# Kernel tuning notes

Hardware: AMD Instinct MI355X
Metric: run time of the kernel (lower is better)

## Reference

```python
import jax, jax.numpy as jnp
import numpy as np

N, E, D, OUT, H, R = 50000, 800000, 64, 64, 4, 32
NEG_SLOPE = 0.2  # GATConv default negative_slope


def setup_inputs() -> dict:
    key = jax.random.key(0)
    ks = jax.random.split(key, 10)
    s = 0.05
    return {
        "x": jax.random.normal(ks[0], (N, D), jnp.float32),
        "edge_index": jax.random.randint(ks[1], (2, E), 0, N, jnp.int32),
        "edge_type": jax.random.randint(ks[2], (E,), 0, R, jnp.int32),
        "rel_emb": jax.random.normal(ks[3], (R, D), jnp.float32) * s,   # nn.Embedding weight
        "W": jax.random.normal(ks[4], (D, H * OUT), jnp.float32) * s,   # GATConv.lin (no bias)
        "W_e": jax.random.normal(ks[5], (D, H * OUT), jnp.float32) * s, # GATConv.lin_edge
        "att_src": jax.random.normal(ks[6], (H, OUT), jnp.float32) * s,
        "att_dst": jax.random.normal(ks[7], (H, OUT), jnp.float32) * s,
        "att_edge": jax.random.normal(ks[8], (H, OUT), jnp.float32) * s,
        "bias": jnp.zeros((OUT,), jnp.float32),
    }


def reference(x, edge_index, edge_type, rel_emb, W, W_e, att_src, att_dst, att_edge, bias):
    src, dst = edge_index[0], edge_index[1]
    # per-head node transform: [N, H, C]
    xh = (x @ W).reshape(N, H, OUT)
    a_src = jnp.einsum("nhc,hc->nh", xh, att_src)  # [N, H]
    a_dst = jnp.einsum("nhc,hc->nh", xh, att_dst)  # [N, H]
    # relational edge embedding lookup + edge transform: [E, H, C]
    eh = (rel_emb[edge_type] @ W_e).reshape(E, H, OUT)
    a_edge = jnp.einsum("ehc,hc->eh", eh, att_edge)  # [E, H]
    # raw attention logits per edge, per head
    alpha = jax.nn.leaky_relu(a_src[src] + a_dst[dst] + a_edge, NEG_SLOPE)
    # segment softmax over incoming edges of each destination node
    m = jax.ops.segment_max(alpha, dst, num_segments=N)
    ex = jnp.exp(alpha - m[dst])
    denom = jax.ops.segment_sum(ex, dst, num_segments=N)
    att = ex / denom[dst]  # [E, H]  (dropout disabled: eval mode)
    # weighted scatter-aggregate of source features
    out = jax.ops.segment_sum(xh[src] * att[:, :, None], dst, num_segments=N)  # [N, H, C]
    # concat=False -> mean over heads, then bias
    return out.mean(axis=1) + bias
```

## Files before the change

### kernel.cpp

```cpp
#include <hip/hip_runtime.h>
#include <hip/hip_fp16.h>

#define N_NODES 50000
#define N_EDGES 800000
#define NREL 32
#define NEG_SLOPE 0.2f
#define SCAN_NB ((N_NODES + 255) / 256)
#define HIST_NB ((N_EDGES + 255) / 256)
#define NXB 256
#define NTILES (N_NODES / 16)

typedef _Float16 f16x8 __attribute__((ext_vector_type(8)));
typedef float f32x4 __attribute__((ext_vector_type(4)));

__global__ __launch_bounds__(64) void prep_kernel(
    const float* __restrict__ rel_emb, const float* __restrict__ W_e,
    const float* __restrict__ att_edge, float* __restrict__ a_edge_r,
    const float* __restrict__ W, const float* __restrict__ att_src,
    const float* __restrict__ att_dst, float* __restrict__ vsd)
{
    int tid = threadIdx.x;
    if (blockIdx.x < NREL) {
        int r = blockIdx.x;
        int h = tid >> 4;
        int i16 = tid & 15;
        float rr = rel_emb[r * 64 + tid];
        float4 acc = {0.f, 0.f, 0.f, 0.f};
        #pragma unroll
        for (int k = 0; k < 64; ++k) {
            float rv = __shfl(rr, k);
            float4 wv = *(const float4*)(W_e + k * 256 + h * 64 + i16 * 4);
            acc.x += rv * wv.x; acc.y += rv * wv.y;
            acc.z += rv * wv.z; acc.w += rv * wv.w;
        }
        float4 aev = *(const float4*)(att_edge + h * 64 + i16 * 4);
        float ae = acc.x * aev.x + acc.y * aev.y + acc.z * aev.z + acc.w * aev.w;
        #pragma unroll
        for (int m = 8; m >= 1; m >>= 1) ae += __shfl_xor(ae, m);
        if (i16 == 0) a_edge_r[r * 4 + h] = ae;
    } else {
        int col8 = blockIdx.x - NREL;
        int h = col8 >> 1;
        const float* att = (col8 & 1) ? att_dst : att_src;
        int k = tid;
        float s = 0.f;
        #pragma unroll 8
        for (int c = 0; c < 64; ++c)
            s += W[k * 256 + h * 64 + c] * att[h * 64 + c];
        vsd[col8 * 64 + k] = s;
    }
}

__global__ __launch_bounds__(256) void nx_mfma(
    const float* __restrict__ x, const float* __restrict__ W,
    const float* __restrict__ vsd, __half* __restrict__ xh,
    float* __restrict__ a_src, float* __restrict__ a_dst)
{
    __shared__ __align__(16) _Float16 Wl[272][72];
    int tid = threadIdx.x;

    for (int idx = tid; idx < 64 * 256; idx += 256) {
        int k = idx >> 8, col = idx & 255;
        Wl[col][k] = (_Float16)W[idx];
    }
    for (int idx = tid; idx < 64 * 16; idx += 256) {
        int k = idx >> 4, col8 = idx & 15;
        Wl[256 + col8][k] = (_Float16)((col8 < 8) ? vsd[col8 * 64 + k] : 0.f);
    }
    __syncthreads();

    int lane = tid & 63;
    int wv = tid >> 6;
    int r16 = lane & 15;
    int kg = lane >> 4;

    for (int tile = blockIdx.x * 4 + wv; tile < NTILES; tile += NXB * 4) {
        int nb = tile * 16;
        const float* __restrict__ xrow = x + (size_t)(nb + r16) * 64 + kg * 8;
        float4 u0 = *(const float4*)(xrow);
        float4 u1 = *(const float4*)(xrow + 4);
        float4 u2 = *(const float4*)(xrow + 32);
        float4 u3 = *(const float4*)(xrow + 36);
        f16x8 A0, A1;
        A0[0] = (_Float16)u0.x; A0[1] = (_Float16)u0.y;
        A0[2] = (_Float16)u0.z; A0[3] = (_Float16)u0.w;
        A0[4] = (_Float16)u1.x; A0[5] = (_Float16)u1.y;
        A0[6] = (_Float16)u1.z; A0[7] = (_Float16)u1.w;
        A1[0] = (_Float16)u2.x; A1[1] = (_Float16)u2.y;
        A1[2] = (_Float16)u2.z; A1[3] = (_Float16)u2.w;
        A1[4] = (_Float16)u3.x; A1[5] = (_Float16)u3.y;
        A1[6] = (_Float16)u3.z; A1[7] = (_Float16)u3.w;

        f32x4 D[17];
        #pragma unroll
        for (int ct = 0; ct < 17; ++ct) {
            f16x8 B0 = *(const f16x8*)&Wl[ct * 16 + r16][kg * 8];
            f16x8 B1 = *(const f16x8*)&Wl[ct * 16 + r16][32 + kg * 8];
            f32x4 d = {0.f, 0.f, 0.f, 0.f};
            d = __builtin_amdgcn_mfma_f32_16x16x32_f16(A0, B0, d, 0, 0, 0);
            d = __builtin_amdgcn_mfma_f32_16x16x32_f16(A1, B1, d, 0, 0, 0);
            D[ct] = d;
        }

        #pragma unroll
        for (int r = 0; r < 4; ++r) {
            int n = nb + kg * 4 + r;
            #pragma unroll
            for (int j = 0; j < 4; ++j) {
                __half2 lo = __floats2half2_rn(D[j][r], D[j + 4][r]);
                __half2 hi = __floats2half2_rn(D[j + 8][r], D[j + 12][r]);
                uint2 pk;
                pk.x = *(unsigned int*)&lo;
                pk.y = *(unsigned int*)&hi;
                *(uint2*)(xh + (size_t)n * 256 + (j * 16 + r16) * 4) = pk;
            }
            if (r16 < 8) {
                float v = D[16][r];
                int h = r16 >> 1;
                if (r16 & 1) a_dst[n * 4 + h] = v;
                else         a_src[n * 4 + h] = v;
            }
        }
    }
}

__global__ __launch_bounds__(256) void hist_kernel(const int* __restrict__ ei,
                                                   int* __restrict__ counts,
                                                   int* __restrict__ rank) {
    int e = blockIdx.x * 256 + threadIdx.x;
    if (e < N_EDGES) rank[e] = atomicAdd(&counts[ei[N_EDGES + e]], 1);
}

__global__ __launch_bounds__(256) void scan1_kernel(const int* __restrict__ counts,
                                                    int* __restrict__ offsets,
                                                    int* __restrict__ blocksums) {
    __shared__ int sh[256];
    int tid = threadIdx.x;
    int i = blockIdx.x * 256 + tid;
    int v = (i < N_NODES) ? counts[i] : 0;
    sh[tid] = v;
    __syncthreads();
    #pragma unroll
    for (int off = 1; off < 256; off <<= 1) {
        int t = (tid >= off) ? sh[tid - off] : 0;
        __syncthreads();
        sh[tid] += t;
        __syncthreads();
    }
    if (i < N_NODES) offsets[i] = sh[tid] - v;
    if (tid == 255) blocksums[blockIdx.x] = sh[255];
}

__global__ __launch_bounds__(256) void scan23_kernel(int* __restrict__ offsets,
                                                     const int* __restrict__ blocksums) {
    __shared__ int wsum[4];
    int tid = threadIdx.x;
    int lane = tid & 63;
    int warp = tid >> 6;

    int v = (tid < SCAN_NB && tid < (int)blockIdx.x) ? blocksums[tid] : 0;
    #pragma unroll
    for (int m = 32; m >= 1; m >>= 1) v += __shfl_xor(v, m);
    if (lane == 0) wsum[warp] = v;
    __syncthreads();
    int boff = wsum[0] + wsum[1] + wsum[2] + wsum[3];

    int i = blockIdx.x * 256 + tid;
    if (i < N_NODES) offsets[i] += boff;
}

__global__ __launch_bounds__(256) void scatter_kernel(const int* __restrict__ ei,
                                                      const int* __restrict__ etype,
                                                      const int* __restrict__ offsets,
                                                      const int* __restrict__ rank,
                                                      int* __restrict__ elist) {
    int e = blockIdx.x * 256 + threadIdx.x;
    if (e >= N_EDGES) return;
    int s = ei[e];
    int d = ei[N_EDGES + e];
    int t = etype[e];
    int pos = offsets[d] + rank[e];
    elist[pos] = (s << 5) | t;
}

__global__ __launch_bounds__(256) void aggregate(
    const int* __restrict__ offsets, const int* __restrict__ counts,
    const int* __restrict__ elist, const float* __restrict__ a_src,
    const float* __restrict__ a_dst, const float* __restrict__ a_edge_r,
    const __half* __restrict__ xh, const float* __restrict__ bias,
    float* __restrict__ out)
{
    __shared__ float4 exsh[4][64];
    __shared__ int    ssh[4][64];
    __shared__ float4 pnum[4][64];
    __shared__ float4 pden[4][64];

    int lane = threadIdx.x & 63;
    int warp = threadIdx.x >> 6;
    int pair = warp >> 1;
    int half = warp & 1;
    int d = blockIdx.x * 2 + pair;

    int beg = offsets[d];
    int deg = counts[d];
    int h1 = (deg + 1) >> 1;
    int mybeg = beg + (half ? h1 : 0);
    int mydeg = half ? (deg - h1) : h1;

    float4 advec = ((const float4*)a_dst)[d];

    float n0 = 0.f, n1 = 0.f, n2 = 0.f, n3 = 0.f;
    float d0 = 0.f, d1 = 0.f, d2 = 0.f, d3 = 0.f;

    for (int base = 0; base < mydeg; base += 64) {
        int m = mydeg - base; if (m > 64) m = 64;

        float4 ev = make_float4(0.f, 0.f, 0.f, 0.f);
        int s = 0;
        if (lane < m) {
            int pk = elist[mybeg + base + lane];
            s = pk >> 5;
            int t = pk & 31;
            float4 as = ((const float4*)a_src)[s];
            float4 ae = ((const float4*)a_edge_r)[t];
            float b0 = as.x + advec.x + ae.x; b0 = b0 > 0.f ? b0 : NEG_SLOPE * b0;
            float b1 = as.y + advec.y + ae.y; b1 = b1 > 0.f ? b1 : NEG_SLOPE * b1;
            float b2 = as.z + advec.z + ae.z; b2 = b2 > 0.f ? b2 : NEG_SLOPE * b2;
            float b3 = as.w + advec.w + ae.w; b3 = b3 > 0.f ? b3 : NEG_SLOPE * b3;
            ev.x = __expf(b0); ev.y = __expf(b1);
            ev.z = __expf(b2); ev.w = __expf(b3);
        }
        d0 += ev.x; d1 += ev.y; d2 += ev.z; d3 += ev.w;
        exsh[warp][lane] = ev;
        ssh[warp][lane]  = s;

        #pragma unroll 4
        for (int j = 0; j < m; ++j) {
            float4 e = exsh[warp][j];
            int sj = ssh[warp][j];
            const __half2* __restrict__ xr =
                (const __half2*)(xh + (size_t)sj * 256 + lane * 4);
            __half2 p0 = xr[0], p1 = xr[1];
            float2 f0 = __half22float2(p0), f1 = __half22float2(p1);
            n0 = fmaf(e.x, f0.x, n0);
            n1 = fmaf(e.y, f0.y, n1);
            n2 = fmaf(e.z, f1.x, n2);
            n3 = fmaf(e.w, f1.y, n3);
        }
    }

    pnum[warp][lane] = make_float4(n0, n1, n2, n3);
    pden[warp][lane] = make_float4(d0, d1, d2, d3);
    __syncthreads();

    if (half == 0) {
        float4 on = pnum[warp + 1][lane];
        float4 od = pden[warp + 1][lane];
        n0 += on.x; n1 += on.y; n2 += on.z; n3 += on.w;
        d0 += od.x; d1 += od.y; d2 += od.z; d3 += od.w;

        #pragma unroll
        for (int msk = 32; msk >= 1; msk >>= 1) {
            d0 += __shfl_xor(d0, msk);
            d1 += __shfl_xor(d1, msk);
            d2 += __shfl_xor(d2, msk);
            d3 += __shfl_xor(d3, msk);
        }

        float r = 0.f;
        if (deg > 0)
            r = 0.25f * (n0 / d0 + n1 / d1 + n2 / d2 + n3 / d3);
        out[(size_t)d * 64 + lane] = r + bias[lane];
    }
}

extern "C" void kernel_launch(void* const* d_in, const int* in_sizes, int n_in,
                              void* d_out, int out_size, void* d_ws, size_t ws_size,
                              hipStream_t stream) {
    const float* x        = (const float*)d_in[0];
    const int*   ei       = (const int*)  d_in[1];
    const int*   etype    = (const int*)  d_in[2];
    const float* rel_emb  = (const float*)d_in[3];
    const float* W        = (const float*)d_in[4];
    const float* W_e      = (const float*)d_in[5];
    const float* att_src  = (const float*)d_in[6];
    const float* att_dst  = (const float*)d_in[7];
    const float* att_edge = (const float*)d_in[8];
    const float* bias     = (const float*)d_in[9];
    float* out = (float*)d_out;

    char* ws = (char*)d_ws;
    __half* xh      = (__half*)ws;
    char* p = ws + (size_t)N_NODES * 256 * 2;
    int*   counts   = (int*)p;                p += N_NODES * 4;
    float* a_src    = (float*)p;              p += N_NODES * 4 * 4;
    float* a_dst    = (float*)p;              p += N_NODES * 4 * 4;
    float* a_edge_r = (float*)p;              p += NREL * 4 * 4;
    float* vsd      = (float*)p;              p += 8 * 64 * 4;
    int*   offsets  = (int*)p;                p += N_NODES * 4;
    int*   blocksums= (int*)p;                p += 256 * 4;
    int*   rank     = (int*)p;                p += (size_t)N_EDGES * 4;
    int*   elist    = (int*)p;                p += (size_t)N_EDGES * 4;

    hipMemsetAsync(counts, 0, N_NODES * sizeof(int), stream);
    prep_kernel<<<NREL + 8, 64, 0, stream>>>(rel_emb, W_e, att_edge, a_edge_r,
                                             W, att_src, att_dst, vsd);
    nx_mfma<<<NXB, 256, 0, stream>>>(x, W, vsd, xh, a_src, a_dst);
    hist_kernel<<<HIST_NB, 256, 0, stream>>>(ei, counts, rank);
    scan1_kernel<<<SCAN_NB, 256, 0, stream>>>(counts, offsets, blocksums);
    scan23_kernel<<<SCAN_NB, 256, 0, stream>>>(offsets, blocksums);
    scatter_kernel<<<HIST_NB, 256, 0, stream>>>(ei, etype, offsets, rank, elist);
    aggregate<<<N_NODES / 2, 256, 0, stream>>>(offsets, counts, elist, a_src,
                                               a_dst, a_edge_r, xh, bias, out);
}
```

Before: 153.2 us.

## Merge prep, node transform and histogram into one heterogeneous kernel

```diff
diff --git a/kernel.cpp b/kernel.cpp
--- a/kernel.cpp
+++ b/kernel.cpp
@@ -13,59 +13,59 @@
 typedef _Float16 f16x8 __attribute__((ext_vector_type(8)));
 typedef float f32x4 __attribute__((ext_vector_type(4)));
 
-__global__ __launch_bounds__(64) void prep_kernel(
+__global__ __launch_bounds__(256) void mega_kernel(
+    const float* __restrict__ x, const float* __restrict__ W,
+    const float* __restrict__ att_src, const float* __restrict__ att_dst,
+    __half* __restrict__ xh, float* __restrict__ a_src, float* __restrict__ a_dst,
+    const int* __restrict__ ei, int* __restrict__ counts, int* __restrict__ rank,
     const float* __restrict__ rel_emb, const float* __restrict__ W_e,
-    const float* __restrict__ att_edge, float* __restrict__ a_edge_r,
-    const float* __restrict__ W, const float* __restrict__ att_src,
-    const float* __restrict__ att_dst, float* __restrict__ vsd)
+    const float* __restrict__ att_edge, float* __restrict__ a_edge_r)
 {
+    __shared__ __align__(16) _Float16 Wl[272][72];
     int tid = threadIdx.x;
-    if (blockIdx.x < NREL) {
-        int r = blockIdx.x;
-        int h = tid >> 4;
-        int i16 = tid & 15;
-        float rr = rel_emb[r * 64 + tid];
-        float4 acc = {0.f, 0.f, 0.f, 0.f};
-        #pragma unroll
-        for (int k = 0; k < 64; ++k) {
-            float rv = __shfl(rr, k);
-            float4 wv = *(const float4*)(W_e + k * 256 + h * 64 + i16 * 4);
-            acc.x += rv * wv.x; acc.y += rv * wv.y;
-            acc.z += rv * wv.z; acc.w += rv * wv.w;
-        }
-        float4 aev = *(const float4*)(att_edge + h * 64 + i16 * 4);
-        float ae = acc.x * aev.x + acc.y * aev.y + acc.z * aev.z + acc.w * aev.w;
-        #pragma unroll
-        for (int m = 8; m >= 1; m >>= 1) ae += __shfl_xor(ae, m);
-        if (i16 == 0) a_edge_r[r * 4 + h] = ae;
-    } else {
-        int col8 = blockIdx.x - NREL;
+    int bid = blockIdx.x;
+
+    if (bid >= NXB) {
+        if (bid < NXB + HIST_NB) {
+            int e = (bid - NXB) * 256 + tid;
+            if (e < N_EDGES) rank[e] = atomicAdd(&counts[ei[N_EDGES + e]], 1);
+        } else if (tid < 64) {
+            int r = bid - (NXB + HIST_NB);
+            int h = tid >> 4;
+            int i16 = tid & 15;
+            float rr = rel_emb[r * 64 + tid];
+            float4 acc = {0.f, 0.f, 0.f, 0.f};
+            #pragma unroll
+            for (int k = 0; k < 64; ++k) {
+                float rv = __shfl(rr, k);
+                float4 wv = *(const float4*)(W_e + k * 256 + h * 64 + i16 * 4);
+                acc.x += rv * wv.x; acc.y += rv * wv.y;
+                acc.z += rv * wv.z; acc.w += rv * wv.w;
+            }
+            float4 aev = *(const float4*)(att_edge + h * 64 + i16 * 4);
+            float ae = acc.x * aev.x + acc.y * aev.y + acc.z * aev.z + acc.w * aev.w;
+            #pragma unroll
+            for (int m = 8; m >= 1; m >>= 1) ae += __shfl_xor(ae, m);
+            if (i16 == 0) a_edge_r[r * 4 + h] = ae;
+        }
+        return;
+    }
+
+    for (int idx = tid; idx < 64 * 256; idx += 256) {
+        int k = idx >> 8, col = idx & 255;
+        Wl[col][k] = (_Float16)W[idx];
+    }
+    for (int idx = tid; idx < 512; idx += 256) {
+        int k = idx & 63;
+        int col8 = idx >> 6;
         int h = col8 >> 1;
         const float* att = (col8 & 1) ? att_dst : att_src;
-        int k = tid;
         float s = 0.f;
         #pragma unroll 8
         for (int c = 0; c < 64; ++c)
             s += W[k * 256 + h * 64 + c] * att[h * 64 + c];
-        vsd[col8 * 64 + k] = s;
-    }
-}
-
-__global__ __launch_bounds__(256) void nx_mfma(
-    const float* __restrict__ x, const float* __restrict__ W,
-    const float* __restrict__ vsd, __half* __restrict__ xh,
-    float* __restrict__ a_src, float* __restrict__ a_dst)
-{
-    __shared__ __align__(16) _Float16 Wl[272][72];
-    int tid = threadIdx.x;
-
-    for (int idx = tid; idx < 64 * 256; idx += 256) {
-        int k = idx >> 8, col = idx & 255;
-        Wl[col][k] = (_Float16)W[idx];
-    }
-    for (int idx = tid; idx < 64 * 16; idx += 256) {
-        int k = idx >> 4, col8 = idx & 15;
-        Wl[256 + col8][k] = (_Float16)((col8 < 8) ? vsd[col8 * 64 + k] : 0.f);
+        Wl[256 + col8][k] = (_Float16)s;
+        Wl[264 + col8][k] = (_Float16)0.f;
     }
     __syncthreads();
 
@@ -74,7 +74,7 @@
     int r16 = lane & 15;
     int kg = lane >> 4;
 
-    for (int tile = blockIdx.x * 4 + wv; tile < NTILES; tile += NXB * 4) {
+    for (int tile = bid * 4 + wv; tile < NTILES; tile += NXB * 4) {
         int nb = tile * 16;
         const float* __restrict__ xrow = x + (size_t)(nb + r16) * 64 + kg * 8;
         float4 u0 = *(const float4*)(xrow);
@@ -124,13 +124,6 @@
     }
 }
 
-__global__ __launch_bounds__(256) void hist_kernel(const int* __restrict__ ei,
-                                                   int* __restrict__ counts,
-                                                   int* __restrict__ rank) {
-    int e = blockIdx.x * 256 + threadIdx.x;
-    if (e < N_EDGES) rank[e] = atomicAdd(&counts[ei[N_EDGES + e]], 1);
-}
-
 __global__ __launch_bounds__(256) void scan1_kernel(const int* __restrict__ counts,
                                                     int* __restrict__ offsets,
                                                     int* __restrict__ blocksums) {
@@ -296,17 +289,15 @@
     float* a_src    = (float*)p;              p += N_NODES * 4 * 4;
     float* a_dst    = (float*)p;              p += N_NODES * 4 * 4;
     float* a_edge_r = (float*)p;              p += NREL * 4 * 4;
-    float* vsd      = (float*)p;              p += 8 * 64 * 4;
     int*   offsets  = (int*)p;                p += N_NODES * 4;
     int*   blocksums= (int*)p;                p += 256 * 4;
     int*   rank     = (int*)p;                p += (size_t)N_EDGES * 4;
     int*   elist    = (int*)p;                p += (size_t)N_EDGES * 4;
 
     hipMemsetAsync(counts, 0, N_NODES * sizeof(int), stream);
-    prep_kernel<<<NREL + 8, 64, 0, stream>>>(rel_emb, W_e, att_edge, a_edge_r,
-                                             W, att_src, att_dst, vsd);
-    nx_mfma<<<NXB, 256, 0, stream>>>(x, W, vsd, xh, a_src, a_dst);
-    hist_kernel<<<HIST_NB, 256, 0, stream>>>(ei, counts, rank);
+    mega_kernel<<<NXB + HIST_NB + NREL, 256, 0, stream>>>(
+        x, W, att_src, att_dst, xh, a_src, a_dst,
+        ei, counts, rank, rel_emb, W_e, att_edge, a_edge_r);
     scan1_kernel<<<SCAN_NB, 256, 0, stream>>>(counts, offsets, blocksums);
     scan23_kernel<<<SCAN_NB, 256, 0, stream>>>(offsets, blocksums);
     scatter_kernel<<<HIST_NB, 256, 0, stream>>>(ei, etype, offsets, rank, elist);
```

Measured after the change: 147.5 us (median of 2 runs). 1.04x faster.
